# Kernel tuning notes

Hardware: AMD Instinct MI355X
Metric: run time of the kernel (lower is better)

Reference implementation:

```python
import jax, jax.numpy as jnp
import numpy as np

EMBED_DIM = 2048
NUM_HEADS = 32
NUM_KV_HEADS = 8
HEAD_DIM = EMBED_DIM // NUM_HEADS  # 64
GROUPS = NUM_HEADS // NUM_KV_HEADS  # 4
BSZ, SEQ = 1, 2048


def apply_rope(x, cos, sin):
    # x: [b, s, h, d]; cos/sin: [s, d//2]. Interleaved-pair (view_as_complex) convention.
    x1 = x[..., 0::2]
    x2 = x[..., 1::2]
    c = cos[None, :, None, :]
    s = sin[None, :, None, :]
    o1 = x1 * c - x2 * s
    o2 = x1 * s + x2 * c
    return jnp.stack([o1, o2], axis=-1).reshape(x.shape)


def setup_inputs() -> dict:
    key = jax.random.key(0)
    ks = jax.random.split(key, 10)
    sc = 1.0 / np.sqrt(EMBED_DIM)
    return {
        "query_states": jax.random.normal(ks[0], (BSZ, SEQ, EMBED_DIM), jnp.float32),
        "key_value_states": jax.random.normal(ks[1], (BSZ, SEQ, EMBED_DIM), jnp.float32),
        "cos_q": jax.random.uniform(ks[2], (SEQ, HEAD_DIM // 2), jnp.float32),
        "sin_q": jax.random.uniform(ks[3], (SEQ, HEAD_DIM // 2), jnp.float32),
        "cos_k": jax.random.uniform(ks[4], (SEQ, HEAD_DIM // 2), jnp.float32),
        "sin_k": jax.random.uniform(ks[5], (SEQ, HEAD_DIM // 2), jnp.float32),
        "attention_mask": jnp.ones((BSZ, SEQ), dtype=bool),
        "wq": jax.random.normal(ks[6], (EMBED_DIM, EMBED_DIM), jnp.float32) * sc,
        "wk": jax.random.normal(ks[7], (NUM_KV_HEADS * HEAD_DIM, EMBED_DIM), jnp.float32) * sc,
        "wv": jax.random.normal(ks[8], (NUM_KV_HEADS * HEAD_DIM, EMBED_DIM), jnp.float32) * sc,
        "wo": jax.random.normal(ks[9], (EMBED_DIM, EMBED_DIM), jnp.float32) * sc,
    }


def reference(query_states, key_value_states, cos_q, sin_q, cos_k, sin_k,
              attention_mask, wq, wk, wv, wo):
    b, ql, _ = query_states.shape
    _, kl, _ = key_value_states.shape
    # Projections (torch Linear, no bias: x @ W.T)
    q = jnp.einsum('bsd,od->bso', query_states, wq).reshape(b, ql, NUM_HEADS, HEAD_DIM)
    k = jnp.einsum('bsd,od->bso', key_value_states, wk).reshape(b, kl, NUM_KV_HEADS, HEAD_DIM)
    v = jnp.einsum('bsd,od->bso', key_value_states, wv).reshape(b, kl, NUM_KV_HEADS, HEAD_DIM)
    q = apply_rope(q, cos_q, sin_q)
    k = apply_rope(k, cos_k, sin_k)
    # GQA without materializing expanded K/V: q heads grouped as (g, kv_head)
    # torch's unsqueeze(2).expand.reshape maps head h -> kv head h % NUM_KV_HEADS,
    # with group index g = h // NUM_KV_HEADS.
    qg = q.transpose(0, 2, 1, 3).reshape(b, GROUPS, NUM_KV_HEADS, ql, HEAD_DIM)
    kt = k.transpose(0, 2, 1, 3)  # [b, kvh, kl, d]
    vt = v.transpose(0, 2, 1, 3)
    scale = 1.0 / jnp.sqrt(jnp.asarray(HEAD_DIM, q.dtype))
    scores = jnp.einsum('bgkqd,bksd->bgkqs', qg, kt) * scale  # [b,g,kvh,ql,kl]
    neg = jnp.asarray(jnp.finfo(scores.dtype).min, scores.dtype)
    scores = jnp.where(attention_mask[:, None, None, None, :], scores, neg)
    probs = jax.nn.softmax(scores, axis=-1)
    out = jnp.einsum('bgkqs,bksd->bgkqd', probs, vt)  # [b,g,kvh,ql,d]
    out = out.reshape(b, NUM_HEADS, ql, HEAD_DIM).transpose(0, 2, 1, 3).reshape(b, ql, NUM_HEADS * HEAD_DIM)
    return jnp.einsum('bso,do->bsd', out, wo)
```

## Files before the change

kernel.cpp:

```cpp
#include <hip/hip_runtime.h>
#include <cstdint>

#define SEQ 2048
#define ED  2048
#define NHEADS 32
#define NKV 8
#define HD 64
#define KVD 512

typedef __attribute__((ext_vector_type(8))) short short8;
typedef __attribute__((ext_vector_type(8))) unsigned short ushort8;
typedef __attribute__((ext_vector_type(4))) float f32x4;

__device__ __forceinline__ float bf2f(unsigned short u){ return __uint_as_float(((unsigned)u)<<16); }
__device__ __forceinline__ unsigned short f2bf(float f){
  unsigned x = __float_as_uint(f);
  return (unsigned short)((x + 0x7fffu + ((x>>16)&1u)) >> 16);
}

__device__ __forceinline__ void gld_lds16(const void* g, void* l){
  __builtin_amdgcn_global_load_lds((const __attribute__((address_space(1))) unsigned*)g,
                                   (__attribute__((address_space(3))) unsigned*)l, 16, 0, 0);
}

__global__ __launch_bounds__(256) void cvt_all(const float* __restrict__ Xq, const float* __restrict__ Xkv,
                                               const float* __restrict__ wq, const float* __restrict__ wk,
                                               const float* __restrict__ wv, const float* __restrict__ wo,
                                               unsigned short* __restrict__ Xb, unsigned short* __restrict__ KVb,
                                               unsigned short* __restrict__ Wqb, unsigned short* __restrict__ WKVb,
                                               unsigned short* __restrict__ Wob){
  int b = blockIdx.x;
  const float* src; unsigned short* dst;
  if (b < 2048)      { src = Xq;  dst = Xb; }
  else if (b < 4096) { src = Xkv; dst = KVb;  b -= 2048; }
  else if (b < 6144) { src = wq;  dst = Wqb;  b -= 4096; }
  else if (b < 6656) { src = wk;  dst = WKVb; b -= 6144; }
  else if (b < 7168) { src = wv;  dst = WKVb + (size_t)512*ED; b -= 6656; }
  else               { src = wo;  dst = Wob;  b -= 7168; }
  size_t t = (size_t)b*256 + threadIdx.x;
  const f32x4* p = (const f32x4*)src + t*2;
  f32x4 a = p[0], c = p[1];
  ushort8 o;
  o[0]=f2bf(a[0]); o[1]=f2bf(a[1]); o[2]=f2bf(a[2]); o[3]=f2bf(a[3]);
  o[4]=f2bf(c[0]); o[5]=f2bf(c[1]); o[6]=f2bf(c[2]); o[7]=f2bf(c[3]);
  *(ushort8*)(dst + t*8) = o;
}

__global__ __launch_bounds__(256) void rope_all(unsigned short* __restrict__ Qb, unsigned short* __restrict__ Kbuf,
                                                const float* __restrict__ cq, const float* __restrict__ sq,
                                                const float* __restrict__ ck, const float* __restrict__ sk){
  int b = blockIdx.x;
  unsigned short* buf; const float* cosT; const float* sinT; int lw; float scale;
  if (b < 2048){ buf=Qb; cosT=cq; sinT=sq; lw=11; scale=0.125f*1.44269504088896f; }
  else { b -= 2048; buf=Kbuf; cosT=ck; sinT=sk; lw=9; scale=1.0f; }
  int t = b*256 + threadIdx.x;
  int e = t*8;
  int s = e >> lw;
  int col = e & ((1<<lw)-1);
  int i0 = (col & 63) >> 1;
  ushort8 v = *(ushort8*)(buf + e);
  f32x4 c  = *(const f32x4*)(cosT + s*32 + i0);
  f32x4 sn = *(const f32x4*)(sinT + s*32 + i0);
  ushort8 o;
#pragma unroll
  for(int p=0;p<4;p++){
    float x1 = bf2f(v[2*p]), x2 = bf2f(v[2*p+1]);
    o[2*p]   = f2bf((x1*c[p] - x2*sn[p])*scale);
    o[2*p+1] = f2bf((x1*sn[p] + x2*c[p])*scale);
  }
  *(ushort8*)(buf + e) = o;
}

template<int EPI>
__device__ __forceinline__ void gemm_body(const unsigned short* __restrict__ A,
                                          const unsigned short* __restrict__ B,
                                          void* __restrict__ Cout, void* __restrict__ Cout2,
                                          int M, int N, int K, int bx, int by,
                                          unsigned short* As, unsigned short* Bs){
  const int tid = threadIdx.x;
  const int lane = tid & 63;
  const int wave = tid >> 6;
  const int wr = wave >> 1, wc = wave & 1;
  const int m0 = by * 128, n0 = bx * 128;
  const int l15 = lane & 15, l4 = lane >> 4;

  f32x4 acc[4][4] = {};

  const int arow0 = tid>>2,        sc0 = tid&3, oc0 = sc0 ^ ((arow0>>1) & 3);
  const int arow1 = (tid+256)>>2,  oc1 = sc0 ^ ((arow1>>1) & 3);
  const unsigned short* Ag0 = A + (size_t)(m0+arow0)*K + oc0*8;
  const unsigned short* Ag1 = A + (size_t)(m0+arow1)*K + oc1*8;
  const unsigned short* Bg0 = B + (size_t)(n0+arow0)*K + oc0*8;
  const unsigned short* Bg1 = B + (size_t)(n0+arow1)*K + oc1*8;

  const int nk = K >> 5;

#define GSTAGE(buf_, kt_) { \
    const int ko_ = (kt_)*32; const int bo_ = (buf_)*4096; \
    gld_lds16(Ag0 + ko_, As + bo_ + tid*8); \
    gld_lds16(Ag1 + ko_, As + bo_ + (tid+256)*8); \
    gld_lds16(Bg0 + ko_, Bs + bo_ + tid*8); \
    gld_lds16(Bg1 + ko_, Bs + bo_ + (tid+256)*8); }

  GSTAGE(0, 0);
  GSTAGE(1, 1);

  for(int kt=0; kt<nk; kt++){
    if (kt+1 == nk) { asm volatile("s_waitcnt vmcnt(0)" ::: "memory"); }
    else            { asm volatile("s_waitcnt vmcnt(4)" ::: "memory"); }
    __builtin_amdgcn_s_barrier();
    __builtin_amdgcn_sched_barrier(0);

    if (kt+2 < nk) GSTAGE((kt+2)%3, kt+2);

    const int cur = (kt%3)*4096;
    short8 af[4], bfr[4];
#pragma unroll
    for(int m=0;m<4;m++){
      int row = wr*64 + m*16 + l15;
      af[m] = *(const short8*)&As[cur + row*32 + ((l4 ^ ((row>>1)&3))*8)];
    }
#pragma unroll
    for(int n=0;n<4;n++){
      int row = wc*64 + n*16 + l15;
      bfr[n] = *(const short8*)&Bs[cur + row*32 + ((l4 ^ ((row>>1)&3))*8)];
    }
    __builtin_amdgcn_s_setprio(1);
#pragma unroll
    for(int m=0;m<4;m++)
#pragma unroll
      for(int n=0;n<4;n++)
        acc[m][n] = __builtin_amdgcn_mfma_f32_16x16x32_bf16(af[m], bfr[n], acc[m][n], 0,0,0);
    __builtin_amdgcn_s_setprio(0);
  }
#undef GSTAGE

#pragma unroll
  for(int m=0;m<4;m++){
    const int row0 = m0 + wr*64 + m*16 + l4*4;
#pragma unroll
    for(int n=0;n<4;n++){
      const int col = n0 + wc*64 + n*16 + l15;
      if constexpr (EPI == 0){
        unsigned short* C = (unsigned short*)Cout;
#pragma unroll
        for(int r=0;r<4;r++) C[(size_t)(row0+r)*N + col] = f2bf(acc[m][n][r]);
      } else if constexpr (EPI == 2){
        float* C = (float*)Cout;
#pragma unroll
        for(int r=0;r<4;r++) C[(size_t)(row0+r)*N + col] = acc[m][n][r];
      } else {
        if (n0 < 512){
          unsigned short* C = (unsigned short*)Cout;
#pragma unroll
          for(int r=0;r<4;r++) C[(size_t)(row0+r)*512 + col] = f2bf(acc[m][n][r]);
        } else {
          unsigned short* C = (unsigned short*)Cout2;
          const int d = col - 512;
#pragma unroll
          for(int r=0;r<4;r++){
            int seq = row0 + r;
            int pos = ((seq>>5)&1)*32 + (seq&15)*2 + ((seq>>4)&1);
            C[(size_t)d*SEQ + (seq & ~63) + pos] = f2bf(acc[m][n][r]);
          }
        }
      }
    }
  }
}

__global__ __launch_bounds__(256) void gemm_proj(const unsigned short* __restrict__ Xb,
                                                 const unsigned short* __restrict__ Wqb,
                                                 const unsigned short* __restrict__ KVb,
                                                 const unsigned short* __restrict__ WKVb,
                                                 unsigned short* __restrict__ Qb,
                                                 unsigned short* __restrict__ Kb,
                                                 unsigned short* __restrict__ Vtb){
  __shared__ unsigned short As[3*4096];
  __shared__ unsigned short Bs[3*4096];
  int b = blockIdx.x;
  if (b < 256){
    gemm_body<0>(Xb, Wqb, Qb, nullptr, SEQ, ED, ED, b&15, b>>4, As, Bs);
  } else {
    int bb = b - 256;
    gemm_body<3>(KVb, WKVb, Kb, Vtb, SEQ, 1024, ED, bb&7, bb>>3, As, Bs);
  }
}

__global__ __launch_bounds__(256) void gemm_out_k(const unsigned short* __restrict__ Obf,
                                                  const unsigned short* __restrict__ Wob,
                                                  float* __restrict__ out){
  __shared__ unsigned short As[3*4096];
  __shared__ unsigned short Bs[3*4096];
  int b = blockIdx.x;
  gemm_body<2>(Obf, Wob, out, nullptr, SEQ, ED, ED, b&15, b>>4, As, Bs);
}

__global__ __launch_bounds__(256) void attn_k(const unsigned short* __restrict__ Qb,
                                              const unsigned short* __restrict__ Kb,
                                              const unsigned short* __restrict__ Vt,
                                              unsigned short* __restrict__ Ob){
  __shared__ unsigned short Ks[2][4096];
  __shared__ unsigned short Vs[2][4096];
  __shared__ unsigned Psu[4][1024];
  const int tid = threadIdx.x, lane = tid & 63, w = tid >> 6;
  const int l15 = lane & 15, l4 = lane >> 4;
  const int qb = blockIdx.x, h = blockIdx.y, kvh = h & 7;

  const int row = tid>>3, sc = tid&7, oc = sc ^ (row&7);
  const int row2 = row + 32, oc2 = sc ^ (row2&7);
  const unsigned short* Kg0 = Kb + (size_t)row*KVD  + kvh*HD + oc*8;
  const unsigned short* Kg1 = Kb + (size_t)row2*KVD + kvh*HD + oc2*8;
  const unsigned short* Vg0 = Vt + (size_t)(kvh*HD+row)*SEQ  + oc*8;
  const unsigned short* Vg1 = Vt + (size_t)(kvh*HD+row2)*SEQ + oc2*8;

#define ATTN_STAGE(buf, kb_) { \
    const size_t koff = (size_t)(kb_)*64*KVD; const int voff = (kb_)*64; \
    gld_lds16(Kg0 + koff, &Ks[buf][tid*8]); \
    gld_lds16(Kg1 + koff, &Ks[buf][(tid+256)*8]); \
    gld_lds16(Vg0 + voff, &Vs[buf][tid*8]); \
    gld_lds16(Vg1 + voff, &Vs[buf][(tid+256)*8]); }

  ATTN_STAGE(0, 0);

  short8 qa[2][2];
  {
    const unsigned short* qp0 = Qb + (size_t)(qb*128 + w*32 + l15)*ED + h*HD + l4*8;
    qa[0][0] = *(const short8*)qp0;
    qa[0][1] = *(const short8*)(qp0 + 32);
    const unsigned short* qp1 = qp0 + (size_t)16*ED;
    qa[1][0] = *(const short8*)qp1;
    qa[1][1] = *(const short8*)(qp1 + 32);
  }

  unsigned* Pw = &Psu[w][0];
  f32x4 o_acc[2][4] = {};
  float l_acc[2][4] = {{0.f,0.f,0.f,0.f},{0.f,0.f,0.f,0.f}};
  __syncthreads();

  for(int kb=0; kb<SEQ/64; kb++){
    const int cur = kb & 1;
    if (kb+1 < SEQ/64) ATTN_STAGE(cur^1, kb+1);

    __builtin_amdgcn_s_setprio(1);
    f32x4 s_acc[2][4] = {};
#pragma unroll
    for(int n=0;n<4;n++){
      int key = n*16 + l15;
#pragma unroll
      for(int ks=0;ks<2;ks++){
        short8 kf = *(const short8*)&Ks[cur][key*64 + (((ks*4+l4) ^ (key&7))*8)];
        s_acc[0][n] = __builtin_amdgcn_mfma_f32_16x16x32_bf16(qa[0][ks], kf, s_acc[0][n], 0,0,0);
        s_acc[1][n] = __builtin_amdgcn_mfma_f32_16x16x32_bf16(qa[1][ks], kf, s_acc[1][n], 0,0,0);
      }
    }
    __builtin_amdgcn_s_setprio(0);

#pragma unroll
    for(int mt=0;mt<2;mt++){
#pragma unroll
      for(int r=0;r<4;r++){
        float p0 = exp2f(s_acc[mt][0][r]), p1 = exp2f(s_acc[mt][1][r]);
        float p2 = exp2f(s_acc[mt][2][r]), p3 = exp2f(s_acc[mt][3][r]);
        l_acc[mt][r] += (p0+p1)+(p2+p3);
        unsigned u01, u23;
        asm("v_cvt_pk_bf16_f32 %0, %1, %2" : "=v"(u01) : "v"(p0), "v"(p1));
        asm("v_cvt_pk_bf16_f32 %0, %1, %2" : "=v"(u23) : "v"(p2), "v"(p3));
        const int q32 = mt*16 + l4*4 + r;
        Pw[q32*32 + (((l15>>2)     ^ (q32&7))<<2) + (l15&3)] = u01;
        Pw[q32*32 + (((4+(l15>>2)) ^ (q32&7))<<2) + (l15&3)] = u23;
      }
    }
    asm volatile("s_waitcnt lgkmcnt(0)" ::: "memory");

    __builtin_amdgcn_s_setprio(1);
#pragma unroll
    for(int ks=0;ks<2;ks++){
      short8 pa0 = *(const short8*)&Pw[(l15     )*32 + (((ks*4+l4) ^ (l15&7))<<2)];
      short8 pa1 = *(const short8*)&Pw[(16+l15  )*32 + (((ks*4+l4) ^ (l15&7))<<2)];
#pragma unroll
      for(int n=0;n<4;n++){
        int d = n*16 + l15;
        short8 vf = *(const short8*)&Vs[cur][d*64 + (((ks*4+l4) ^ (d&7))*8)];
        o_acc[0][n] = __builtin_amdgcn_mfma_f32_16x16x32_bf16(pa0, vf, o_acc[0][n], 0,0,0);
        o_acc[1][n] = __builtin_amdgcn_mfma_f32_16x16x32_bf16(pa1, vf, o_acc[1][n], 0,0,0);
      }
    }
    __builtin_amdgcn_s_setprio(0);
    __syncthreads();
  }
#undef ATTN_STAGE

#pragma unroll
  for(int mt=0;mt<2;mt++)
#pragma unroll
    for(int r=0;r<4;r++){
      float t = l_acc[mt][r];
      t += __shfl_xor(t,1); t += __shfl_xor(t,2); t += __shfl_xor(t,4); t += __shfl_xor(t,8);
      l_acc[mt][r] = 1.0f / t;
    }
#pragma unroll
  for(int mt=0;mt<2;mt++)
#pragma unroll
    for(int n=0;n<4;n++){
      const int col = h*HD + n*16 + l15;
#pragma unroll
      for(int r=0;r<4;r++){
        const int srow = qb*128 + w*32 + mt*16 + l4*4 + r;
        Ob[(size_t)srow*ED + col] = f2bf(o_acc[mt][n][r] * l_acc[mt][r]);
      }
    }
}

extern "C" void kernel_launch(void* const* d_in, const int* in_sizes, int n_in,
                              void* d_out, int out_size, void* d_ws, size_t ws_size,
                              hipStream_t stream) {
  const float* Xq    = (const float*)d_in[0];
  const float* Xkv   = (const float*)d_in[1];
  const float* cos_q = (const float*)d_in[2];
  const float* sin_q = (const float*)d_in[3];
  const float* cos_k = (const float*)d_in[4];
  const float* sin_k = (const float*)d_in[5];
  const float* wq = (const float*)d_in[7];
  const float* wk = (const float*)d_in[8];
  const float* wv = (const float*)d_in[9];
  const float* wo = (const float*)d_in[10];
  float* out = (float*)d_out;

  char* ws = (char*)d_ws;
  const size_t MB = 1u<<20;
  unsigned short* Xb   = (unsigned short*)(ws + 0*MB);
  unsigned short* KVb  = (unsigned short*)(ws + 8*MB);
  unsigned short* Wqb  = (unsigned short*)(ws + 16*MB);
  unsigned short* WKVb = (unsigned short*)(ws + 24*MB);
  unsigned short* Wob  = (unsigned short*)(ws + 28*MB);
  unsigned short* Qb   = (unsigned short*)(ws + 36*MB);
  unsigned short* Kb   = (unsigned short*)(ws + 44*MB);
  unsigned short* Vtb  = (unsigned short*)(ws + 46*MB);
  unsigned short* Obf  = (unsigned short*)(ws + 48*MB);

  cvt_all<<<9216,256,0,stream>>>(Xq, Xkv, wq, wk, wv, wo, Xb, KVb, Wqb, WKVb, Wob);

  gemm_proj<<<384,256,0,stream>>>(Xb, Wqb, KVb, WKVb, Qb, Kb, Vtb);

  rope_all<<<2560,256,0,stream>>>(Qb, Kb, cos_q, sin_q, cos_k, sin_k);

  attn_k<<<dim3(SEQ/128, NHEADS),256,0,stream>>>(Qb, Kb, Vtb, Obf);

  gemm_out_k<<<256,256,0,stream>>>(Obf, Wob, out);
}
```

Measured before the change: 283.7 us.

## Split-K the GEMMs and split-KV attention, fuse RoPE into projection epilogue

The projection and output GEMMs are split into two K halves. Each half writes a partial result, and the last-arriving block (found through an atomic flag) reduces both halves. For the projection GEMM that block also applies RoPE and the softmax scale, so the separate rope kernel is gone. Attention is split into two halves of the KV sequence, with a flag-based combine of the partial outputs and row sums, and it uses a raw v_exp_f32. The goal is more blocks to fill the CUs and fewer launches, at the cost of extra partial-buffer traffic, threadfence/atomic overhead and a memset of the flags.

```diff
diff --git a/kernel.cpp b/kernel.cpp
--- a/kernel.cpp
+++ b/kernel.cpp
@@ -12,31 +12,32 @@
 typedef __attribute__((ext_vector_type(8))) unsigned short ushort8;
 typedef __attribute__((ext_vector_type(4))) float f32x4;
 
+#define QSCALE (0.125f*1.44269504088896f)
+
 __device__ __forceinline__ float bf2f(unsigned short u){ return __uint_as_float(((unsigned)u)<<16); }
 __device__ __forceinline__ unsigned short f2bf(float f){
   unsigned x = __float_as_uint(f);
   return (unsigned short)((x + 0x7fffu + ((x>>16)&1u)) >> 16);
 }
+__device__ __forceinline__ float fexp2(float x){ float r; asm("v_exp_f32 %0, %1":"=v"(r):"v"(x)); return r; }
 
 __device__ __forceinline__ void gld_lds16(const void* g, void* l){
   __builtin_amdgcn_global_load_lds((const __attribute__((address_space(1))) unsigned*)g,
                                    (__attribute__((address_space(3))) unsigned*)l, 16, 0, 0);
 }
 
-__global__ __launch_bounds__(256) void cvt_all(const float* __restrict__ Xq, const float* __restrict__ Xkv,
-                                               const float* __restrict__ wq, const float* __restrict__ wk,
-                                               const float* __restrict__ wv, const float* __restrict__ wo,
-                                               unsigned short* __restrict__ Xb, unsigned short* __restrict__ KVb,
-                                               unsigned short* __restrict__ Wqb, unsigned short* __restrict__ WKVb,
-                                               unsigned short* __restrict__ Wob){
+__global__ __launch_bounds__(256) void cvt_main(const float* __restrict__ Xq, const float* __restrict__ Xkv,
+                                                const float* __restrict__ wq, const float* __restrict__ wk,
+                                                const float* __restrict__ wv,
+                                                unsigned short* __restrict__ Xb, unsigned short* __restrict__ KVb,
+                                                unsigned short* __restrict__ Wqb, unsigned short* __restrict__ WKVb){
   int b = blockIdx.x;
   const float* src; unsigned short* dst;
   if (b < 2048)      { src = Xq;  dst = Xb; }
   else if (b < 4096) { src = Xkv; dst = KVb;  b -= 2048; }
   else if (b < 6144) { src = wq;  dst = Wqb;  b -= 4096; }
   else if (b < 6656) { src = wk;  dst = WKVb; b -= 6144; }
-  else if (b < 7168) { src = wv;  dst = WKVb + (size_t)512*ED; b -= 6656; }
-  else               { src = wo;  dst = Wob;  b -= 7168; }
+  else               { src = wv;  dst = WKVb + (size_t)512*ED; b -= 6656; }
   size_t t = (size_t)b*256 + threadIdx.x;
   const f32x4* p = (const f32x4*)src + t*2;
   f32x4 a = p[0], c = p[1];
@@ -46,54 +47,44 @@
   *(ushort8*)(dst + t*8) = o;
 }
 
-__global__ __launch_bounds__(256) void rope_all(unsigned short* __restrict__ Qb, unsigned short* __restrict__ Kbuf,
-                                                const float* __restrict__ cq, const float* __restrict__ sq,
-                                                const float* __restrict__ ck, const float* __restrict__ sk){
-  int b = blockIdx.x;
-  unsigned short* buf; const float* cosT; const float* sinT; int lw; float scale;
-  if (b < 2048){ buf=Qb; cosT=cq; sinT=sq; lw=11; scale=0.125f*1.44269504088896f; }
-  else { b -= 2048; buf=Kbuf; cosT=ck; sinT=sk; lw=9; scale=1.0f; }
-  int t = b*256 + threadIdx.x;
-  int e = t*8;
-  int s = e >> lw;
-  int col = e & ((1<<lw)-1);
-  int i0 = (col & 63) >> 1;
-  ushort8 v = *(ushort8*)(buf + e);
-  f32x4 c  = *(const f32x4*)(cosT + s*32 + i0);
-  f32x4 sn = *(const f32x4*)(sinT + s*32 + i0);
+__global__ __launch_bounds__(256) void cvt_wo(const float* __restrict__ wo, unsigned short* __restrict__ Wob){
+  size_t t = (size_t)blockIdx.x*256 + threadIdx.x;
+  const f32x4* p = (const f32x4*)wo + t*2;
+  f32x4 a = p[0], c = p[1];
   ushort8 o;
-#pragma unroll
-  for(int p=0;p<4;p++){
-    float x1 = bf2f(v[2*p]), x2 = bf2f(v[2*p+1]);
-    o[2*p]   = f2bf((x1*c[p] - x2*sn[p])*scale);
-    o[2*p+1] = f2bf((x1*sn[p] + x2*c[p])*scale);
-  }
-  *(ushort8*)(buf + e) = o;
+  o[0]=f2bf(a[0]); o[1]=f2bf(a[1]); o[2]=f2bf(a[2]); o[3]=f2bf(a[3]);
+  o[4]=f2bf(c[0]); o[5]=f2bf(c[1]); o[6]=f2bf(c[2]); o[7]=f2bf(c[3]);
+  *(ushort8*)(Wob + t*8) = o;
 }
 
 template<int EPI>
-__device__ __forceinline__ void gemm_body(const unsigned short* __restrict__ A,
-                                          const unsigned short* __restrict__ B,
-                                          void* __restrict__ Cout, void* __restrict__ Cout2,
-                                          int M, int N, int K, int bx, int by,
-                                          unsigned short* As, unsigned short* Bs){
+__device__ __forceinline__ void gemm_split(const unsigned short* __restrict__ A,
+                                           const unsigned short* __restrict__ B,
+                                           int bx, int by, int ks, int* __restrict__ flag,
+                                           unsigned short* __restrict__ Pb0, unsigned short* __restrict__ Pb1,
+                                           float* __restrict__ Pf,
+                                           unsigned short* __restrict__ F0, unsigned short* __restrict__ F1,
+                                           float* __restrict__ Fout,
+                                           const float* __restrict__ cosT, const float* __restrict__ sinT,
+                                           unsigned short* As, unsigned short* Bs, int* who_s){
   const int tid = threadIdx.x;
   const int lane = tid & 63;
   const int wave = tid >> 6;
   const int wr = wave >> 1, wc = wave & 1;
   const int m0 = by * 128, n0 = bx * 128;
   const int l15 = lane & 15, l4 = lane >> 4;
+  const int kbase = ks * (ED/2);
 
   f32x4 acc[4][4] = {};
 
   const int arow0 = tid>>2,        sc0 = tid&3, oc0 = sc0 ^ ((arow0>>1) & 3);
   const int arow1 = (tid+256)>>2,  oc1 = sc0 ^ ((arow1>>1) & 3);
-  const unsigned short* Ag0 = A + (size_t)(m0+arow0)*K + oc0*8;
-  const unsigned short* Ag1 = A + (size_t)(m0+arow1)*K + oc1*8;
-  const unsigned short* Bg0 = B + (size_t)(n0+arow0)*K + oc0*8;
-  const unsigned short* Bg1 = B + (size_t)(n0+arow1)*K + oc1*8;
-
-  const int nk = K >> 5;
+  const unsigned short* Ag0 = A + (size_t)(m0+arow0)*ED + kbase + oc0*8;
+  const unsigned short* Ag1 = A + (size_t)(m0+arow1)*ED + kbase + oc1*8;
+  const unsigned short* Bg0 = B + (size_t)(n0+arow0)*ED + kbase + oc0*8;
+  const unsigned short* Bg1 = B + (size_t)(n0+arow1)*ED + kbase + oc1*8;
+
+  const int nk = (ED/2) >> 5;
 
 #define GSTAGE(buf_, kt_) { \
     const int ko_ = (kt_)*32; const int bo_ = (buf_)*4096; \
@@ -141,28 +132,75 @@
 #pragma unroll
     for(int n=0;n<4;n++){
       const int col = n0 + wc*64 + n*16 + l15;
+      if constexpr (EPI == 2){
+        float* P = Pf + (size_t)ks*SEQ*ED;
+#pragma unroll
+        for(int r=0;r<4;r++) P[(size_t)(row0+r)*ED + col] = acc[m][n][r];
+      } else if constexpr (EPI == 0){
+        unsigned short* P = Pb0 + (size_t)ks*SEQ*ED;
+#pragma unroll
+        for(int r=0;r<4;r++) P[(size_t)(row0+r)*ED + col] = f2bf(acc[m][n][r]);
+      } else {
+        const bool isK = (n0 < 512);
+        unsigned short* P = (isK ? Pb0 : Pb1) + (size_t)ks*SEQ*KVD;
+        const int cp = col - (isK ? 0 : 512);
+#pragma unroll
+        for(int r=0;r<4;r++) P[(size_t)(row0+r)*KVD + cp] = f2bf(acc[m][n][r]);
+      }
+    }
+  }
+
+  __threadfence();
+  __syncthreads();
+  if (tid == 0) *who_s = atomicAdd(flag, 1);
+  __syncthreads();
+  if (!*who_s) return;
+  __threadfence();
+
+#pragma unroll
+  for(int m=0;m<4;m++){
+    const int row0 = m0 + wr*64 + m*16 + l4*4;
+#pragma unroll
+    for(int n=0;n<4;n++){
+      const int col = n0 + wc*64 + n*16 + l15;
       if constexpr (EPI == 0){
-        unsigned short* C = (unsigned short*)Cout;
-#pragma unroll
-        for(int r=0;r<4;r++) C[(size_t)(row0+r)*N + col] = f2bf(acc[m][n][r]);
-      } else if constexpr (EPI == 2){
-        float* C = (float*)Cout;
-#pragma unroll
-        for(int r=0;r<4;r++) C[(size_t)(row0+r)*N + col] = acc[m][n][r];
+        const unsigned short* Po = Pb0 + (size_t)(ks^1)*SEQ*ED;
+#pragma unroll
+        for(int r=0;r<4;r++){
+          const int row = row0 + r;
+          float x = bf2f(f2bf(acc[m][n][r])) + bf2f(Po[(size_t)row*ED + col]);
+          float xo = __shfl_xor(x, 1);
+          const int jh = (col & 63) >> 1;
+          float cc = cosT[row*32 + jh], ss = sinT[row*32 + jh];
+          float res = (l15 & 1) ? fmaf(xo, ss, x*cc) : (x*cc - xo*ss);
+          F0[(size_t)row*ED + col] = f2bf(res * QSCALE);
+        }
+      } else if constexpr (EPI == 1){
+        const bool isK = (n0 < 512);
+        const unsigned short* Po = (isK ? Pb0 : Pb1) + (size_t)(ks^1)*SEQ*KVD;
+        const int cp = col - (isK ? 0 : 512);
+#pragma unroll
+        for(int r=0;r<4;r++){
+          const int row = row0 + r;
+          float x = bf2f(f2bf(acc[m][n][r])) + bf2f(Po[(size_t)row*KVD + cp]);
+          if (isK){
+            float xo = __shfl_xor(x, 1);
+            const int jh = (col & 63) >> 1;
+            float cc = cosT[row*32 + jh], ss = sinT[row*32 + jh];
+            float res = (l15 & 1) ? fmaf(xo, ss, x*cc) : (x*cc - xo*ss);
+            F0[(size_t)row*KVD + col] = f2bf(res);
+          } else {
+            const int seq = row;
+            const int pos = ((seq>>5)&1)*32 + (seq&15)*2 + ((seq>>4)&1);
+            F1[(size_t)cp*SEQ + (seq & ~63) + pos] = f2bf(x);
+          }
+        }
       } else {
-        if (n0 < 512){
-          unsigned short* C = (unsigned short*)Cout;
-#pragma unroll
-          for(int r=0;r<4;r++) C[(size_t)(row0+r)*512 + col] = f2bf(acc[m][n][r]);
-        } else {
-          unsigned short* C = (unsigned short*)Cout2;
-          const int d = col - 512;
-#pragma unroll
-          for(int r=0;r<4;r++){
-            int seq = row0 + r;
-            int pos = ((seq>>5)&1)*32 + (seq&15)*2 + ((seq>>4)&1);
-            C[(size_t)d*SEQ + (seq & ~63) + pos] = f2bf(acc[m][n][r]);
-          }
+        const float* Po = Pf + (size_t)(ks^1)*SEQ*ED;
+#pragma unroll
+        for(int r=0;r<4;r++){
+          const int row = row0 + r;
+          Fout[(size_t)row*ED + col] = acc[m][n][r] + Po[(size_t)row*ED + col];
         }
       }
     }
@@ -173,39 +211,59 @@
                                                  const unsigned short* __restrict__ Wqb,
                                                  const unsigned short* __restrict__ KVb,
                                                  const unsigned short* __restrict__ WKVb,
+                                                 unsigned short* __restrict__ Qp,
+                                                 unsigned short* __restrict__ Kp,
+                                                 unsigned short* __restrict__ Vp,
                                                  unsigned short* __restrict__ Qb,
                                                  unsigned short* __restrict__ Kb,
-                                                 unsigned short* __restrict__ Vtb){
+                                                 unsigned short* __restrict__ Vtb,
+                                                 int* __restrict__ flags,
+                                                 const float* __restrict__ cq, const float* __restrict__ sq,
+                                                 const float* __restrict__ ck, const float* __restrict__ sk){
   __shared__ unsigned short As[3*4096];
   __shared__ unsigned short Bs[3*4096];
+  __shared__ int who_s;
   int b = blockIdx.x;
-  if (b < 256){
-    gemm_body<0>(Xb, Wqb, Qb, nullptr, SEQ, ED, ED, b&15, b>>4, As, Bs);
+  if (b < 512){
+    int ks = b >> 8, t = b & 255;
+    gemm_split<0>(Xb, Wqb, t&15, t>>4, ks, flags + t,
+                  Qp, nullptr, nullptr, Qb, nullptr, nullptr, cq, sq, As, Bs, &who_s);
   } else {
-    int bb = b - 256;
-    gemm_body<3>(KVb, WKVb, Kb, Vtb, SEQ, 1024, ED, bb&7, bb>>3, As, Bs);
+    int bb = b - 512;
+    int ks = bb >> 7, t = bb & 127;
+    gemm_split<1>(KVb, WKVb, t&7, t>>3, ks, flags + 256 + t,
+                  Kp, Vp, nullptr, Kb, Vtb, nullptr, ck, sk, As, Bs, &who_s);
   }
 }
 
 __global__ __launch_bounds__(256) void gemm_out_k(const unsigned short* __restrict__ Obf,
                                                   const unsigned short* __restrict__ Wob,
-                                                  float* __restrict__ out){
+                                                  float* __restrict__ Op,
+                                                  float* __restrict__ out,
+                                                  int* __restrict__ flags){
   __shared__ unsigned short As[3*4096];
   __shared__ unsigned short Bs[3*4096];
+  __shared__ int who_s;
   int b = blockIdx.x;
-  gemm_body<2>(Obf, Wob, out, nullptr, SEQ, ED, ED, b&15, b>>4, As, Bs);
+  int ks = b >> 8, t = b & 255;
+  gemm_split<2>(Obf, Wob, t&15, t>>4, ks, flags + 1024 + t,
+                nullptr, nullptr, Op, nullptr, nullptr, out, nullptr, nullptr, As, Bs, &who_s);
 }
 
 __global__ __launch_bounds__(256) void attn_k(const unsigned short* __restrict__ Qb,
                                               const unsigned short* __restrict__ Kb,
                                               const unsigned short* __restrict__ Vt,
-                                              unsigned short* __restrict__ Ob){
+                                              float* __restrict__ Oa,
+                                              float* __restrict__ La,
+                                              unsigned short* __restrict__ Ob,
+                                              int* __restrict__ flags){
   __shared__ unsigned short Ks[2][4096];
   __shared__ unsigned short Vs[2][4096];
   __shared__ unsigned Psu[4][1024];
+  __shared__ int who_s;
   const int tid = threadIdx.x, lane = tid & 63, w = tid >> 6;
   const int l15 = lane & 15, l4 = lane >> 4;
-  const int qb = blockIdx.x, h = blockIdx.y, kvh = h & 7;
+  const int qb = blockIdx.x, h = blockIdx.y, z = blockIdx.z, kvh = h & 7;
 
   const int row = tid>>3, sc = tid&7, oc = sc ^ (row&7);
   const int row2 = row + 32, oc2 = sc ^ (row2&7);
@@ -221,7 +279,8 @@
     gld_lds16(Vg0 + voff, &Vs[buf][tid*8]); \
     gld_lds16(Vg1 + voff, &Vs[buf][(tid+256)*8]); }
 
-  ATTN_STAGE(0, 0);
+  const int kb0 = z*16;
+  ATTN_STAGE(0, kb0);
 
   short8 qa[2][2];
   {
@@ -238,9 +297,9 @@
   float l_acc[2][4] = {{0.f,0.f,0.f,0.f},{0.f,0.f,0.f,0.f}};
   __syncthreads();
 
-  for(int kb=0; kb<SEQ/64; kb++){
-    const int cur = kb & 1;
-    if (kb+1 < SEQ/64) ATTN_STAGE(cur^1, kb+1);
+  for(int i=0; i<16; i++){
+    const int cur = i & 1;
+    if (i+1 < 16) ATTN_STAGE(cur^1, kb0+i+1);
 
     __builtin_amdgcn_s_setprio(1);
     f32x4 s_acc[2][4] = {};
@@ -260,8 +319,8 @@
     for(int mt=0;mt<2;mt++){
 #pragma unroll
       for(int r=0;r<4;r++){
-        float p0 = exp2f(s_acc[mt][0][r]), p1 = exp2f(s_acc[mt][1][r]);
-        float p2 = exp2f(s_acc[mt][2][r]), p3 = exp2f(s_acc[mt][3][r]);
+        float p0 = fexp2(s_acc[mt][0][r]), p1 = fexp2(s_acc[mt][1][r]);
+        float p2 = fexp2(s_acc[mt][2][r]), p3 = fexp2(s_acc[mt][3][r]);
         l_acc[mt][r] += (p0+p1)+(p2+p3);
         unsigned u01, u23;
         asm("v_cvt_pk_bf16_f32 %0, %1, %2" : "=v"(u01) : "v"(p0), "v"(p1));
@@ -276,8 +335,8 @@
     __builtin_amdgcn_s_setprio(1);
 #pragma unroll
     for(int ks=0;ks<2;ks++){
-      short8 pa0 = *(const short8*)&Pw[(l15     )*32 + (((ks*4+l4) ^ (l15&7))<<2)];
-      short8 pa1 = *(const short8*)&Pw[(16+l15  )*32 + (((ks*4+l4) ^ (l15&7))<<2)];
+      short8 pa0 = *(const short8*)&Pw[(l15   )*32 + (((ks*4+l4) ^ (l15&7))<<2)];
+      short8 pa1 = *(const short8*)&Pw[(16+l15)*32 + (((ks*4+l4) ^ (l15&7))<<2)];
 #pragma unroll
       for(int n=0;n<4;n++){
         int d = n*16 + l15;
@@ -297,8 +356,11 @@
     for(int r=0;r<4;r++){
       float t = l_acc[mt][r];
       t += __shfl_xor(t,1); t += __shfl_xor(t,2); t += __shfl_xor(t,4); t += __shfl_xor(t,8);
-      l_acc[mt][r] = 1.0f / t;
-    }
+      l_acc[mt][r] = t;
+    }
+
+  float* OaZ = Oa + (size_t)z*SEQ*ED;
+  float* LaZ = La + (size_t)z*NHEADS*SEQ + (size_t)h*SEQ;
 #pragma unroll
   for(int mt=0;mt<2;mt++)
 #pragma unroll
@@ -307,7 +369,44 @@
 #pragma unroll
       for(int r=0;r<4;r++){
         const int srow = qb*128 + w*32 + mt*16 + l4*4 + r;
-        Ob[(size_t)srow*ED + col] = f2bf(o_acc[mt][n][r] * l_acc[mt][r]);
+        OaZ[(size_t)srow*ED + col] = o_acc[mt][n][r];
+      }
+    }
+  if (l15 == 0){
+#pragma unroll
+    for(int mt=0;mt<2;mt++)
+#pragma unroll
+      for(int r=0;r<4;r++)
+        LaZ[qb*128 + w*32 + mt*16 + l4*4 + r] = l_acc[mt][r];
+  }
+
+  __threadfence();
+  __syncthreads();
+  if (tid == 0) who_s = atomicAdd(&flags[h*16 + qb], 1);
+  __syncthreads();
+  if (!who_s) return;
+  __threadfence();
+
+  const float* OaO = Oa + (size_t)(z^1)*SEQ*ED;
+  const float* LaO = La + (size_t)(z^1)*NHEADS*SEQ + (size_t)h*SEQ;
+  float inv[2][4];
+#pragma unroll
+  for(int mt=0;mt<2;mt++)
+#pragma unroll
+    for(int r=0;r<4;r++){
+      const int srow = qb*128 + w*32 + mt*16 + l4*4 + r;
+      inv[mt][r] = 1.0f / (l_acc[mt][r] + LaO[srow]);
+    }
+#pragma unroll
+  for(int mt=0;mt<2;mt++)
+#pragma unroll
+    for(int n=0;n<4;n++){
+      const int col = h*HD + n*16 + l15;
+#pragma unroll
+      for(int r=0;r<4;r++){
+        const int srow = qb*128 + w*32 + mt*16 + l4*4 + r;
+        float tot = o_acc[mt][n][r] + OaO[(size_t)srow*ED + col];
+        Ob[(size_t)srow*ED + col] = f2bf(tot * inv[mt][r]);
       }
     }
 }
@@ -329,23 +428,33 @@
 
   char* ws = (char*)d_ws;
   const size_t MB = 1u<<20;
-  unsigned short* Xb   = (unsigned short*)(ws + 0*MB);
-  unsigned short* KVb  = (unsigned short*)(ws + 8*MB);
-  unsigned short* Wqb  = (unsigned short*)(ws + 16*MB);
-  unsigned short* WKVb = (unsigned short*)(ws + 24*MB);
-  unsigned short* Wob  = (unsigned short*)(ws + 28*MB);
-  unsigned short* Qb   = (unsigned short*)(ws + 36*MB);
-  unsigned short* Kb   = (unsigned short*)(ws + 44*MB);
-  unsigned short* Vtb  = (unsigned short*)(ws + 46*MB);
-  unsigned short* Obf  = (unsigned short*)(ws + 48*MB);
-
-  cvt_all<<<9216,256,0,stream>>>(Xq, Xkv, wq, wk, wv, wo, Xb, KVb, Wqb, WKVb, Wob);
-
-  gemm_proj<<<384,256,0,stream>>>(Xb, Wqb, KVb, WKVb, Qb, Kb, Vtb);
-
-  rope_all<<<2560,256,0,stream>>>(Qb, Kb, cos_q, sin_q, cos_k, sin_k);
-
-  attn_k<<<dim3(SEQ/128, NHEADS),256,0,stream>>>(Qb, Kb, Vtb, Obf);
-
-  gemm_out_k<<<256,256,0,stream>>>(Obf, Wob, out);
-}
+  int* flags = (int*)ws;
+  unsigned short* Xb   = (unsigned short*)(ws + 1*MB);
+  unsigned short* KVb  = (unsigned short*)(ws + 9*MB);
+  unsigned short* Wqb  = (unsigned short*)(ws + 17*MB);
+  unsigned short* WKVb = (unsigned short*)(ws + 25*MB);
+  unsigned short* Qp   = (unsigned short*)(ws + 29*MB);
+  unsigned short* Kp   = (unsigned short*)(ws + 45*MB);
+  unsigned short* Vp   = (unsigned short*)(ws + 49*MB);
+  unsigned short* Qb   = (unsigned short*)(ws + 53*MB);
+  unsigned short* Kb   = (unsigned short*)(ws + 61*MB);
+  unsigned short* Vtb  = (unsigned short*)(ws + 63*MB);
+  float*          Oa   = (float*)(ws + 1*MB);
+  float*          La   = (float*)(ws + 33*MB);
+  unsigned short* Obf  = (unsigned short*)(ws + 34*MB);
+  unsigned short* Wob  = (unsigned short*)(ws + 42*MB);
+  float*          Op   = (float*)(ws + 1*MB);
+
+  hipMemsetAsync(ws, 0, 8192, stream);
+
+  cvt_main<<<7168,256,0,stream>>>(Xq, Xkv, wq, wk, wv, Xb, KVb, Wqb, WKVb);
+
+  gemm_proj<<<768,256,0,stream>>>(Xb, Wqb, KVb, WKVb, Qp, Kp, Vp, Qb, Kb, Vtb,
+                                  flags, cos_q, sin_q, cos_k, sin_k);
+
+  cvt_wo<<<2048,256,0,stream>>>(wo, Wob);
+
+  attn_k<<<dim3(SEQ/128, NHEADS, 2),256,0,stream>>>(Qb, Kb, Vtb, Oa, La, Obf, flags + 512);
+
+  gemm_out_k<<<512,256,0,stream>>>(Obf, Wob, Op, out, flags);
+}
```

Result: slower. 717.3 us (+152.8%).

## Halve GEMM M-tile to 64, deepen LDS pipeline to 4 stages, use raw v_exp

Applied to the files above, without the earlier changes.

The GEMM tile shrinks from 128x128 to 64x128, which doubles the grid of the projection and output GEMMs (768 and 512 blocks) so the many CUs on the device have more blocks to run. The LDS ring grows from 3 to 4 stages, prefetching three k-tiles ahead with matching vmcnt waits. In attention, exp2f is replaced by a raw v_exp_f32 instruction to avoid library range handling. The smaller tile lowers arithmetic intensity and re-reads B tiles more often, in exchange for better CU occupancy and load balance.

```diff
diff --git a/kernel.cpp b/kernel.cpp
--- a/kernel.cpp
+++ b/kernel.cpp
@@ -17,6 +17,7 @@
   unsigned x = __float_as_uint(f);
   return (unsigned short)((x + 0x7fffu + ((x>>16)&1u)) >> 16);
 }
+__device__ __forceinline__ float fexp2(float x){ float r; asm("v_exp_f32 %0, %1":"=v"(r):"v"(x)); return r; }
 
 __device__ __forceinline__ void gld_lds16(const void* g, void* l){
   __builtin_amdgcn_global_load_lds((const __attribute__((address_space(1))) unsigned*)g,
@@ -81,53 +82,55 @@
   const int lane = tid & 63;
   const int wave = tid >> 6;
   const int wr = wave >> 1, wc = wave & 1;
-  const int m0 = by * 128, n0 = bx * 128;
+  const int m0 = by * 64, n0 = bx * 128;
   const int l15 = lane & 15, l4 = lane >> 4;
 
-  f32x4 acc[4][4] = {};
-
-  const int arow0 = tid>>2,        sc0 = tid&3, oc0 = sc0 ^ ((arow0>>1) & 3);
-  const int arow1 = (tid+256)>>2,  oc1 = sc0 ^ ((arow1>>1) & 3);
-  const unsigned short* Ag0 = A + (size_t)(m0+arow0)*K + oc0*8;
-  const unsigned short* Ag1 = A + (size_t)(m0+arow1)*K + oc1*8;
-  const unsigned short* Bg0 = B + (size_t)(n0+arow0)*K + oc0*8;
-  const unsigned short* Bg1 = B + (size_t)(n0+arow1)*K + oc1*8;
+  f32x4 acc[2][4] = {};
+
+  const int arow = tid>>2, sc0 = tid&3;
+  const int aoc  = sc0 ^ ((arow>>1)&3);
+  const int brow1 = (tid+256)>>2;
+  const int boc1  = sc0 ^ ((brow1>>1)&3);
+  const unsigned short* Ag  = A + (size_t)(m0+arow)*K  + aoc*8;
+  const unsigned short* Bg0 = B + (size_t)(n0+arow)*K  + aoc*8;
+  const unsigned short* Bg1 = B + (size_t)(n0+brow1)*K + boc1*8;
 
   const int nk = K >> 5;
 
 #define GSTAGE(buf_, kt_) { \
-    const int ko_ = (kt_)*32; const int bo_ = (buf_)*4096; \
-    gld_lds16(Ag0 + ko_, As + bo_ + tid*8); \
-    gld_lds16(Ag1 + ko_, As + bo_ + (tid+256)*8); \
-    gld_lds16(Bg0 + ko_, Bs + bo_ + tid*8); \
-    gld_lds16(Bg1 + ko_, Bs + bo_ + (tid+256)*8); }
+    const int ko_ = (kt_)*32; \
+    gld_lds16(Ag  + ko_, As + (buf_)*2048 + tid*8); \
+    gld_lds16(Bg0 + ko_, Bs + (buf_)*4096 + tid*8); \
+    gld_lds16(Bg1 + ko_, Bs + (buf_)*4096 + (tid+256)*8); }
 
   GSTAGE(0, 0);
   GSTAGE(1, 1);
+  GSTAGE(2, 2);
 
   for(int kt=0; kt<nk; kt++){
-    if (kt+1 == nk) { asm volatile("s_waitcnt vmcnt(0)" ::: "memory"); }
-    else            { asm volatile("s_waitcnt vmcnt(4)" ::: "memory"); }
+    if (kt+1 == nk)      { asm volatile("s_waitcnt vmcnt(0)" ::: "memory"); }
+    else if (kt+2 == nk) { asm volatile("s_waitcnt vmcnt(3)" ::: "memory"); }
+    else                 { asm volatile("s_waitcnt vmcnt(6)" ::: "memory"); }
     __builtin_amdgcn_s_barrier();
     __builtin_amdgcn_sched_barrier(0);
 
-    if (kt+2 < nk) GSTAGE((kt+2)%3, kt+2);
-
-    const int cur = (kt%3)*4096;
-    short8 af[4], bfr[4];
-#pragma unroll
-    for(int m=0;m<4;m++){
-      int row = wr*64 + m*16 + l15;
-      af[m] = *(const short8*)&As[cur + row*32 + ((l4 ^ ((row>>1)&3))*8)];
+    if (kt+3 < nk) GSTAGE((kt+3)&3, kt+3);
+
+    const int curA = (kt&3)*2048, curB = (kt&3)*4096;
+    short8 af[2], bfr[4];
+#pragma unroll
+    for(int m=0;m<2;m++){
+      int row = wr*32 + m*16 + l15;
+      af[m] = *(const short8*)&As[curA + row*32 + ((l4 ^ ((row>>1)&3))*8)];
     }
 #pragma unroll
     for(int n=0;n<4;n++){
       int row = wc*64 + n*16 + l15;
-      bfr[n] = *(const short8*)&Bs[cur + row*32 + ((l4 ^ ((row>>1)&3))*8)];
+      bfr[n] = *(const short8*)&Bs[curB + row*32 + ((l4 ^ ((row>>1)&3))*8)];
     }
     __builtin_amdgcn_s_setprio(1);
 #pragma unroll
-    for(int m=0;m<4;m++)
+    for(int m=0;m<2;m++)
 #pragma unroll
       for(int n=0;n<4;n++)
         acc[m][n] = __builtin_amdgcn_mfma_f32_16x16x32_bf16(af[m], bfr[n], acc[m][n], 0,0,0);
@@ -136,8 +139,8 @@
 #undef GSTAGE
 
 #pragma unroll
-  for(int m=0;m<4;m++){
-    const int row0 = m0 + wr*64 + m*16 + l4*4;
+  for(int m=0;m<2;m++){
+    const int row0 = m0 + wr*32 + m*16 + l4*4;
 #pragma unroll
     for(int n=0;n<4;n++){
       const int col = n0 + wc*64 + n*16 + l15;
@@ -176,13 +179,13 @@
                                                  unsigned short* __restrict__ Qb,
                                                  unsigned short* __restrict__ Kb,
                                                  unsigned short* __restrict__ Vtb){
-  __shared__ unsigned short As[3*4096];
-  __shared__ unsigned short Bs[3*4096];
+  __shared__ unsigned short As[4*2048];
+  __shared__ unsigned short Bs[4*4096];
   int b = blockIdx.x;
-  if (b < 256){
+  if (b < 512){
     gemm_body<0>(Xb, Wqb, Qb, nullptr, SEQ, ED, ED, b&15, b>>4, As, Bs);
   } else {
-    int bb = b - 256;
+    int bb = b - 512;
     gemm_body<3>(KVb, WKVb, Kb, Vtb, SEQ, 1024, ED, bb&7, bb>>3, As, Bs);
   }
 }
@@ -190,8 +193,8 @@
 __global__ __launch_bounds__(256) void gemm_out_k(const unsigned short* __restrict__ Obf,
                                                   const unsigned short* __restrict__ Wob,
                                                   float* __restrict__ out){
-  __shared__ unsigned short As[3*4096];
-  __shared__ unsigned short Bs[3*4096];
+  __shared__ unsigned short As[4*2048];
+  __shared__ unsigned short Bs[4*4096];
   int b = blockIdx.x;
   gemm_body<2>(Obf, Wob, out, nullptr, SEQ, ED, ED, b&15, b>>4, As, Bs);
 }
@@ -260,8 +263,8 @@
     for(int mt=0;mt<2;mt++){
 #pragma unroll
       for(int r=0;r<4;r++){
-        float p0 = exp2f(s_acc[mt][0][r]), p1 = exp2f(s_acc[mt][1][r]);
-        float p2 = exp2f(s_acc[mt][2][r]), p3 = exp2f(s_acc[mt][3][r]);
+        float p0 = fexp2(s_acc[mt][0][r]), p1 = fexp2(s_acc[mt][1][r]);
+        float p2 = fexp2(s_acc[mt][2][r]), p3 = fexp2(s_acc[mt][3][r]);
         l_acc[mt][r] += (p0+p1)+(p2+p3);
         unsigned u01, u23;
         asm("v_cvt_pk_bf16_f32 %0, %1, %2" : "=v"(u01) : "v"(p0), "v"(p1));
@@ -276,8 +279,8 @@
     __builtin_amdgcn_s_setprio(1);
 #pragma unroll
     for(int ks=0;ks<2;ks++){
-      short8 pa0 = *(const short8*)&Pw[(l15     )*32 + (((ks*4+l4) ^ (l15&7))<<2)];
-      short8 pa1 = *(const short8*)&Pw[(16+l15  )*32 + (((ks*4+l4) ^ (l15&7))<<2)];
+      short8 pa0 = *(const short8*)&Pw[(l15   )*32 + (((ks*4+l4) ^ (l15&7))<<2)];
+      short8 pa1 = *(const short8*)&Pw[(16+l15)*32 + (((ks*4+l4) ^ (l15&7))<<2)];
 #pragma unroll
       for(int n=0;n<4;n++){
         int d = n*16 + l15;
@@ -341,11 +344,11 @@
 
   cvt_all<<<9216,256,0,stream>>>(Xq, Xkv, wq, wk, wv, wo, Xb, KVb, Wqb, WKVb, Wob);
 
-  gemm_proj<<<384,256,0,stream>>>(Xb, Wqb, KVb, WKVb, Qb, Kb, Vtb);
+  gemm_proj<<<768,256,0,stream>>>(Xb, Wqb, KVb, WKVb, Qb, Kb, Vtb);
 
   rope_all<<<2560,256,0,stream>>>(Qb, Kb, cos_q, sin_q, cos_k, sin_k);
 
   attn_k<<<dim3(SEQ/128, NHEADS),256,0,stream>>>(Qb, Kb, Vtb, Obf);
 
-  gemm_out_k<<<256,256,0,stream>>>(Obf, Wob, out);
-}
+  gemm_out_k<<<512,256,0,stream>>>(Obf, Wob, out);
+}
```

Measured after the change: 259.3 us. -8.6%, faster.
